# Optimization experiments

Hardware: AMD Instinct MI355X
Metric: run time of the kernel (lower is better)

## Reference

```python
import jax, jax.numpy as jnp
import numpy as np

N_NODES = 100000
N_EDGES = 1600000
IN_DIM = 128
HID_DIM = 128
OUT_DIM = 16
N_GRAPHS = 128


def setup_inputs() -> dict:
    key = jax.random.key(0)
    ks = jax.random.split(key, 8)
    x = jax.random.normal(ks[0], (N_NODES, IN_DIM), dtype=jnp.float32)
    edge_index = jax.random.randint(ks[1], (2, N_EDGES), 0, N_NODES, dtype=jnp.int64)
    batch = jnp.sort(jax.random.randint(ks[2], (N_NODES,), 0, N_GRAPHS, dtype=jnp.int64))
    # GCNConv params (glorot-ish scale) and Linear params
    w1 = jax.random.normal(ks[3], (IN_DIM, HID_DIM), dtype=jnp.float32) / np.sqrt(IN_DIM)
    b1 = jnp.zeros((HID_DIM,), dtype=jnp.float32)
    w2 = jax.random.normal(ks[4], (HID_DIM, HID_DIM), dtype=jnp.float32) / np.sqrt(HID_DIM)
    b2 = jnp.zeros((HID_DIM,), dtype=jnp.float32)
    wc = jax.random.normal(ks[5], (HID_DIM, OUT_DIM), dtype=jnp.float32) / np.sqrt(HID_DIM)
    bc = jnp.zeros((OUT_DIM,), dtype=jnp.float32)
    return {"x": x, "edge_index": edge_index, "batch": batch,
            "w1": w1, "b1": b1, "w2": w2, "b2": b2, "wc": wc, "bc": bc}


def _gcn_layer(h, src, dst, w, b, n_nodes):
    # h: [N, Fin]; src/dst: [E+N] (self-loops already appended)
    h = h @ w  # [N, Fout]
    ones = jnp.ones_like(dst, dtype=h.dtype)
    deg = jax.ops.segment_sum(ones, dst, num_segments=n_nodes)  # [N]
    dinv = jnp.where(deg > 0, jax.lax.rsqrt(deg), 0.0)
    norm = dinv[src] * dinv[dst]  # [E+N]
    msg = h[src] * norm[:, None]  # gather + scale, [E+N, Fout]
    out = jax.ops.segment_sum(msg, dst, num_segments=n_nodes)  # scatter-add
    return out + b


def reference(x, edge_index, batch, w1, b1, w2, b2, wc, bc):
    n = x.shape[0]
    loop = jnp.arange(n, dtype=edge_index.dtype)
    src = jnp.concatenate([edge_index[0], loop])  # add self-loops (PyG default)
    dst = jnp.concatenate([edge_index[1], loop])

    h = jax.nn.relu(_gcn_layer(x, src, dst, w1, b1, n))
    h = jax.nn.relu(_gcn_layer(h, src, dst, w2, b2, n))

    # global mean pool over graphs
    sums = jax.ops.segment_sum(h, batch, num_segments=N_GRAPHS)  # [G, H]
    cnt = jax.ops.segment_sum(jnp.ones((n,), h.dtype), batch, num_segments=N_GRAPHS)
    pooled = sums / jnp.maximum(cnt, 1.0)[:, None]

    return pooled @ wc + bc  # [G, OUT_DIM]
```

## Files before the change

kernel.cpp:

```cpp
#include <hip/hip_runtime.h>
#include <stdint.h>

#define NN 100000
#define NE 1600000
#define FDIM 128
#define NGRAPH 128
#define ODIM 16
#define NBKT 391
#define CAP 4608
#define SCHUNK 4096
#define NSCAT ((NE + SCHUNK - 1) / SCHUNK)

typedef __attribute__((ext_vector_type(8))) short short8;
typedef __attribute__((ext_vector_type(8))) unsigned short ushort8;
typedef __attribute__((ext_vector_type(4))) float f32x4;

__device__ __forceinline__ float blo(unsigned int p) { return __uint_as_float(p << 16); }
__device__ __forceinline__ float bhi(unsigned int p) { return __uint_as_float(p & 0xffff0000u); }
__device__ __forceinline__ unsigned short f2b(float f) {
    unsigned int u = __float_as_uint(f);
    unsigned int r = (u + 0x7fffu + ((u >> 16) & 1u)) >> 16;
    return (unsigned short)r;
}
__device__ __forceinline__ unsigned int packbf(float lo, float hi) {
    return (unsigned int)f2b(lo) | ((unsigned int)f2b(hi) << 16);
}

__device__ __forceinline__ int ld_idx(const int* __restrict__ p, long long i, int w) {
    return w ? p[2 * i] : p[i];
}

__global__ void k_init(const int* __restrict__ ei, int* __restrict__ flag,
                       int* __restrict__ bcursor) {
    __shared__ int s;
    int t = threadIdx.x;
    if (t == 0) s = 0;
    __syncthreads();
    if (t < 64) {
        int v = ei[2 * t + 1];
        if (v != 0) atomicOr(&s, 1);
    }
    if (t < NBKT) bcursor[t] = t * CAP;
    __syncthreads();
    if (t == 0) *flag = (s == 0) ? 1 : 0;
}

__global__ void __launch_bounds__(512) k_scat(const int* __restrict__ ei,
                                              int* __restrict__ bcursor,
                                              unsigned int* __restrict__ rec,
                                              const int* __restrict__ flag) {
    __shared__ int hist[NBKT];
    __shared__ int gcur[NBKT];
    int t = threadIdx.x;
    for (int i = t; i < NBKT; i += 512) hist[i] = 0;
    __syncthreads();
    int w = *flag;
    long long e0 = (long long)blockIdx.x * SCHUNK;
    unsigned int myrec[8];
    int mybkt[8];
    #pragma unroll
    for (int j = 0; j < 8; ++j) {
        long long e = e0 + j * 512 + t;
        if (e < NE) {
            int s = ld_idx(ei, e, w);
            int d = ld_idx(ei, NE + e, w);
            mybkt[j] = d >> 8;
            myrec[j] = (unsigned int)s | ((unsigned int)(d & 255) << 17);
            atomicAdd(&hist[mybkt[j]], 1);
        } else mybkt[j] = -1;
    }
    __syncthreads();
    for (int i = t; i < NBKT; i += 512) {
        int c = hist[i];
        if (c) gcur[i] = atomicAdd(&bcursor[i], c);
    }
    __syncthreads();
    #pragma unroll
    for (int j = 0; j < 8; ++j) {
        int b = mybkt[j];
        if (b >= 0) {
            int p = atomicAdd(&gcur[b], 1);
            if (p < (b + 1) * CAP) rec[p] = myrec[j];
        }
    }
}

__global__ void __launch_bounds__(256) k_bucket(const unsigned int* __restrict__ rec,
                                                const int* __restrict__ bcursor,
                                                int* __restrict__ csr,
                                                int* __restrict__ offs,
                                                int* __restrict__ deg,
                                                float* __restrict__ dinv) {
    __shared__ unsigned int rbuf[CAP];
    __shared__ int srcout[CAP];
    __shared__ int hist[256], scn[256], cur[256];
    int b = blockIdx.x, t = threadIdx.x;
    int base = b * CAP;
    int cnt = bcursor[b] - base;
    if (cnt > CAP) cnt = CAP;
    hist[t] = 0;
    __syncthreads();
    for (int j = t; j < cnt; j += 256) {
        unsigned int r = rec[base + j];
        rbuf[j] = r;
        atomicAdd(&hist[r >> 17], 1);
    }
    __syncthreads();
    int v = hist[t];
    scn[t] = v;
    __syncthreads();
    for (int o = 1; o < 256; o <<= 1) {
        int tv = (t >= o) ? scn[t - o] : 0;
        __syncthreads();
        scn[t] += tv;
        __syncthreads();
    }
    int excl = scn[t] - v;
    cur[t] = excl;
    int node = (b << 8) + t;
    if (node < NN) {
        offs[node] = base + excl;
        deg[node] = v;
        dinv[node] = rsqrtf((float)(v + 1));
    }
    __syncthreads();
    for (int j = t; j < cnt; j += 256) {
        unsigned int r = rbuf[j];
        int p = atomicAdd(&cur[r >> 17], 1);
        srcout[p] = (int)(r & 0x1FFFFu);
    }
    __syncthreads();
    for (int j = t; j < cnt; j += 256) csr[base + j] = srcout[j];
}

__global__ void k_starts(const int* __restrict__ batch, int* __restrict__ gstart,
                         const int* __restrict__ flag) {
    int i = blockIdx.x * 256 + threadIdx.x;
    if (i >= NN) return;
    int w = *flag;
    int b = ld_idx(batch, i, w);
    int prev = (i == 0) ? -1 : ld_idx(batch, i - 1, w);
    for (int g = prev + 1; g <= b; ++g) gstart[g] = i;
    if (i == NN - 1)
        for (int g = b + 1; g <= NGRAPH; ++g) gstart[g] = NN;
}

__global__ void k_transpose(const float* __restrict__ w1, const float* __restrict__ w2,
                            unsigned short* __restrict__ wt1, unsigned short* __restrict__ wt2) {
    int idx = blockIdx.x * 256 + threadIdx.x;
    int which = idx >> 14, r = idx & 16383;
    int k = r >> 7, j = r & 127;
    const float* w = which ? w2 : w1;
    unsigned short* wt = which ? wt2 : wt1;
    wt[j * 128 + k] = f2b(w[k * 128 + j]);
}

#define LWS 136
template <bool BF16IN>
__global__ void __launch_bounds__(256) k_gemm(
    const void* __restrict__ Xv,
    const unsigned short* __restrict__ WT,
    const float* __restrict__ dinv,
    unsigned short* __restrict__ OUT)
{
    __shared__ unsigned short lw[128 * LWS];
    int tid = threadIdx.x;
    for (int it = 0; it < 8; ++it) {
        int vidx = it * 256 + tid;
        int j = vidx >> 4, kc = vidx & 15;
        ushort8 v = *(const ushort8*)(WT + j * 128 + kc * 8);
        *(ushort8*)(&lw[j * LWS + kc * 8]) = v;
    }
    __syncthreads();

    int wave = tid >> 6, lane = tid & 63;
    int quad = lane >> 4, n16 = lane & 15;
    int row0 = (blockIdx.x * 4 + wave) * 16;
    if (row0 >= NN) return;

    f32x4 acc[8];
    for (int ct = 0; ct < 8; ++ct) acc[ct] = (f32x4){0.f, 0.f, 0.f, 0.f};

    const int arow = row0 + n16;
    for (int kk = 0; kk < 4; ++kk) {
        short8 a;
        if (BF16IN) {
            a = *(const short8*)((const unsigned short*)Xv + (size_t)arow * 128 + kk * 32 + quad * 8);
        } else {
            const float* ap = (const float*)Xv + (size_t)arow * 128 + kk * 32 + quad * 8;
            float4 a01 = *(const float4*)(ap);
            float4 a23 = *(const float4*)(ap + 4);
            a[0] = (short)f2b(a01.x); a[1] = (short)f2b(a01.y);
            a[2] = (short)f2b(a01.z); a[3] = (short)f2b(a01.w);
            a[4] = (short)f2b(a23.x); a[5] = (short)f2b(a23.y);
            a[6] = (short)f2b(a23.z); a[7] = (short)f2b(a23.w);
        }
        for (int ct = 0; ct < 8; ++ct) {
            short8 b = *(const short8*)(&lw[(ct * 16 + n16) * LWS + kk * 32 + quad * 8]);
            acc[ct] = __builtin_amdgcn_mfma_f32_16x16x32_bf16(a, b, acc[ct], 0, 0, 0);
        }
    }
    for (int r = 0; r < 4; ++r) {
        int row = row0 + quad * 4 + r;
        float dv = dinv[row];
        for (int ct = 0; ct < 8; ++ct)
            OUT[(size_t)row * 128 + ct * 16 + n16] = f2b(acc[ct][r] * dv);
    }
}

__global__ void __launch_bounds__(256) k_agg(
    const unsigned short* __restrict__ XWS,
    const int* __restrict__ csr,
    const int* __restrict__ offs,
    const int* __restrict__ deg,
    const float* __restrict__ dinv,
    const float* __restrict__ bias,
    unsigned short* __restrict__ H)
{
    int wave = threadIdx.x >> 6, lane = threadIdx.x & 63;
    int v = blockIdx.x * 4 + wave;
    int g = lane >> 4, f = lane & 15;
    int beg = offs[v], end = beg + deg[v];
    float a[8];
    if (g == 0) {
        uint4 q = *(const uint4*)(XWS + (size_t)v * FDIM + f * 8);
        a[0] = blo(q.x); a[1] = bhi(q.x); a[2] = blo(q.y); a[3] = bhi(q.y);
        a[4] = blo(q.z); a[5] = bhi(q.z); a[6] = blo(q.w); a[7] = bhi(q.w);
    } else {
        #pragma unroll
        for (int i = 0; i < 8; ++i) a[i] = 0.f;
    }
    int j = beg;
    for (; j + 4 <= end; j += 4) {
        int idx = csr[j + g];
        uint4 q = *(const uint4*)(XWS + (size_t)idx * FDIM + f * 8);
        a[0] += blo(q.x); a[1] += bhi(q.x); a[2] += blo(q.y); a[3] += bhi(q.y);
        a[4] += blo(q.z); a[5] += bhi(q.z); a[6] += blo(q.w); a[7] += bhi(q.w);
    }
    int rem = end - j;
    if (g < rem) {
        int idx = csr[j + g];
        uint4 q = *(const uint4*)(XWS + (size_t)idx * FDIM + f * 8);
        a[0] += blo(q.x); a[1] += bhi(q.x); a[2] += blo(q.y); a[3] += bhi(q.y);
        a[4] += blo(q.z); a[5] += bhi(q.z); a[6] += blo(q.w); a[7] += bhi(q.w);
    }
    #pragma unroll
    for (int i = 0; i < 8; ++i) {
        a[i] += __shfl_xor(a[i], 16);
        a[i] += __shfl_xor(a[i], 32);
    }
    if (g == 0) {
        float dv = dinv[v];
        float4 b0 = *(const float4*)(bias + f * 8);
        float4 b1 = *(const float4*)(bias + f * 8 + 4);
        uint4 o;
        o.x = packbf(fmaxf(fmaf(a[0], dv, b0.x), 0.f), fmaxf(fmaf(a[1], dv, b0.y), 0.f));
        o.y = packbf(fmaxf(fmaf(a[2], dv, b0.z), 0.f), fmaxf(fmaf(a[3], dv, b0.w), 0.f));
        o.z = packbf(fmaxf(fmaf(a[4], dv, b1.x), 0.f), fmaxf(fmaf(a[5], dv, b1.y), 0.f));
        o.w = packbf(fmaxf(fmaf(a[6], dv, b1.z), 0.f), fmaxf(fmaf(a[7], dv, b1.w), 0.f));
        *(uint4*)(H + (size_t)v * FDIM + f * 8) = o;
    }
}

__global__ void __launch_bounds__(256) k_pool(
    const unsigned short* __restrict__ H, const int* __restrict__ gstart,
    float* __restrict__ pooled)
{
    __shared__ float red[512];
    int g = blockIdx.x;
    int t = threadIdx.x;
    int pair = t & 63;
    int seg = t >> 6;
    int beg = gstart[g], end = gstart[g + 1];
    float a0 = 0.f, a1 = 0.f;
    for (int i = beg + seg; i < end; i += 4) {
        unsigned int q = *(const unsigned int*)(H + (size_t)i * FDIM + 2 * pair);
        a0 += blo(q); a1 += bhi(q);
    }
    red[t] = a0; red[256 + t] = a1;
    __syncthreads();
    if (seg == 0) {
        a0 = red[t] + red[t + 64] + red[t + 128] + red[t + 192];
        a1 = red[256 + t] + red[256 + t + 64] + red[256 + t + 128] + red[256 + t + 192];
        float inv = 1.f / fmaxf((float)(end - beg), 1.f);
        pooled[g * FDIM + 2 * pair]     = a0 * inv;
        pooled[g * FDIM + 2 * pair + 1] = a1 * inv;
    }
}

__global__ void k_cls(const float* __restrict__ pooled, const float* __restrict__ wc,
                      const float* __restrict__ bcb, float* __restrict__ out)
{
    int idx = blockIdx.x * 256 + threadIdx.x;
    if (idx >= NGRAPH * ODIM) return;
    int g = idx >> 4, o = idx & 15;
    float acc = bcb[o];
    for (int f = 0; f < FDIM; ++f)
        acc += pooled[g * FDIM + f] * wc[f * ODIM + o];
    out[idx] = acc;
}

extern "C" void kernel_launch(void* const* d_in, const int* in_sizes, int n_in,
                              void* d_out, int out_size, void* d_ws, size_t ws_size,
                              hipStream_t stream) {
    const float* x   = (const float*)d_in[0];
    const int* ei    = (const int*)d_in[1];
    const int* batch = (const int*)d_in[2];
    const float* w1  = (const float*)d_in[3];
    const float* b1  = (const float*)d_in[4];
    const float* w2  = (const float*)d_in[5];
    const float* b2  = (const float*)d_in[6];
    const float* wc  = (const float*)d_in[7];
    const float* bc  = (const float*)d_in[8];
    float* out = (float*)d_out;

    char* ws = (char*)d_ws;
    size_t off = 0;
    auto alloc = [&](size_t bytes) -> void* {
        off = (off + 255) & ~(size_t)255;
        void* p = ws + off;
        off += bytes;
        return p;
    };
    int*   flag    = (int*)alloc(4);
    int*   bcursor = (int*)alloc(NBKT * 4);
    int*   offs    = (int*)alloc(NN * 4);
    int*   deg     = (int*)alloc(NN * 4);
    float* dinv    = (float*)alloc(NN * 4);
    int*   gstart  = (int*)alloc((NGRAPH + 1) * 4);
    unsigned int* rec = (unsigned int*)alloc((size_t)NBKT * CAP * 4);
    int*   csr     = (int*)alloc((size_t)NBKT * CAP * 4);
    unsigned short* wt1 = (unsigned short*)alloc(128 * 128 * 2);
    unsigned short* wt2 = (unsigned short*)alloc(128 * 128 * 2);
    float* pooled  = (float*)alloc(NGRAPH * FDIM * 4);
    unsigned short* xws = (unsigned short*)alloc((size_t)NN * FDIM * 2);
    unsigned short* h   = (unsigned short*)alloc((size_t)NN * FDIM * 2);

    k_init<<<1, 512, 0, stream>>>(ei, flag, bcursor);
    k_scat<<<NSCAT, 512, 0, stream>>>(ei, bcursor, rec, flag);
    k_bucket<<<NBKT, 256, 0, stream>>>(rec, bcursor, csr, offs, deg, dinv);
    k_starts<<<(NN + 255) / 256, 256, 0, stream>>>(batch, gstart, flag);
    k_transpose<<<128, 256, 0, stream>>>(w1, w2, wt1, wt2);

    k_gemm<false><<<(NN / 16 + 3) / 4, 256, 0, stream>>>(x, wt1, dinv, xws);
    k_agg<<<NN / 4, 256, 0, stream>>>(xws, csr, offs, deg, dinv, b1, h);
    k_gemm<true><<<(NN / 16 + 3) / 4, 256, 0, stream>>>(h, wt2, dinv, xws);
    k_agg<<<NN / 4, 256, 0, stream>>>(xws, csr, offs, deg, dinv, b2, h);
    k_pool<<<NGRAPH, 256, 0, stream>>>(h, gstart, pooled);
    k_cls<<<8, 256, 0, stream>>>(pooled, wc, bc, out);
}
```

Measured before the change: 365.3 us.

## Split GCN aggregation across feature slices with eight edges per wave

Result: slower. 853.3 us (+133.6%).

```diff
diff --git a/kernel.cpp b/kernel.cpp
--- a/kernel.cpp
+++ b/kernel.cpp
@@ -217,48 +217,34 @@
     const float* __restrict__ bias,
     unsigned short* __restrict__ H)
 {
+    int slice = blockIdx.x & 7;
+    int grp   = blockIdx.x >> 3;
     int wave = threadIdx.x >> 6, lane = threadIdx.x & 63;
-    int v = blockIdx.x * 4 + wave;
-    int g = lane >> 4, f = lane & 15;
+    int v = grp * 4 + wave;
+    int e8 = lane >> 3, dw = lane & 7;
+    int fb = slice * 16 + dw * 2;
     int beg = offs[v], end = beg + deg[v];
-    float a[8];
-    if (g == 0) {
-        uint4 q = *(const uint4*)(XWS + (size_t)v * FDIM + f * 8);
-        a[0] = blo(q.x); a[1] = bhi(q.x); a[2] = blo(q.y); a[3] = bhi(q.y);
-        a[4] = blo(q.z); a[5] = bhi(q.z); a[6] = blo(q.w); a[7] = bhi(q.w);
-    } else {
-        #pragma unroll
-        for (int i = 0; i < 8; ++i) a[i] = 0.f;
-    }
-    int j = beg;
-    for (; j + 4 <= end; j += 4) {
-        int idx = csr[j + g];
-        uint4 q = *(const uint4*)(XWS + (size_t)idx * FDIM + f * 8);
-        a[0] += blo(q.x); a[1] += bhi(q.x); a[2] += blo(q.y); a[3] += bhi(q.y);
-        a[4] += blo(q.z); a[5] += bhi(q.z); a[6] += blo(q.w); a[7] += bhi(q.w);
-    }
-    int rem = end - j;
-    if (g < rem) {
-        int idx = csr[j + g];
-        uint4 q = *(const uint4*)(XWS + (size_t)idx * FDIM + f * 8);
-        a[0] += blo(q.x); a[1] += bhi(q.x); a[2] += blo(q.y); a[3] += bhi(q.y);
-        a[4] += blo(q.z); a[5] += bhi(q.z); a[6] += blo(q.w); a[7] += bhi(q.w);
-    }
-    #pragma unroll
-    for (int i = 0; i < 8; ++i) {
-        a[i] += __shfl_xor(a[i], 16);
-        a[i] += __shfl_xor(a[i], 32);
-    }
-    if (g == 0) {
+    float a0 = 0.f, a1 = 0.f;
+    if (e8 == 0) {
+        unsigned int q = *(const unsigned int*)(XWS + (size_t)v * FDIM + fb);
+        a0 = blo(q); a1 = bhi(q);
+    }
+    for (int j = beg; j < end; j += 8) {
+        int jj = j + e8;
+        if (jj < end) {
+            int idx = csr[jj];
+            unsigned int q = *(const unsigned int*)(XWS + (size_t)idx * FDIM + fb);
+            a0 += blo(q); a1 += bhi(q);
+        }
+    }
+    a0 += __shfl_xor(a0, 8);  a1 += __shfl_xor(a1, 8);
+    a0 += __shfl_xor(a0, 16); a1 += __shfl_xor(a1, 16);
+    a0 += __shfl_xor(a0, 32); a1 += __shfl_xor(a1, 32);
+    if (e8 == 0) {
         float dv = dinv[v];
-        float4 b0 = *(const float4*)(bias + f * 8);
-        float4 b1 = *(const float4*)(bias + f * 8 + 4);
-        uint4 o;
-        o.x = packbf(fmaxf(fmaf(a[0], dv, b0.x), 0.f), fmaxf(fmaf(a[1], dv, b0.y), 0.f));
-        o.y = packbf(fmaxf(fmaf(a[2], dv, b0.z), 0.f), fmaxf(fmaf(a[3], dv, b0.w), 0.f));
-        o.z = packbf(fmaxf(fmaf(a[4], dv, b1.x), 0.f), fmaxf(fmaf(a[5], dv, b1.y), 0.f));
-        o.w = packbf(fmaxf(fmaf(a[6], dv, b1.z), 0.f), fmaxf(fmaf(a[7], dv, b1.w), 0.f));
-        *(uint4*)(H + (size_t)v * FDIM + f * 8) = o;
+        float2 bp = *(const float2*)(bias + fb);
+        *(unsigned int*)(H + (size_t)v * FDIM + fb) =
+            packbf(fmaxf(fmaf(a0, dv, bp.x), 0.f), fmaxf(fmaf(a1, dv, bp.y), 0.f));
     }
 }
 
@@ -343,9 +329,9 @@
     k_transpose<<<128, 256, 0, stream>>>(w1, w2, wt1, wt2);
 
     k_gemm<false><<<(NN / 16 + 3) / 4, 256, 0, stream>>>(x, wt1, dinv, xws);
-    k_agg<<<NN / 4, 256, 0, stream>>>(xws, csr, offs, deg, dinv, b1, h);
+    k_agg<<<(NN / 4) * 8, 256, 0, stream>>>(xws, csr, offs, deg, dinv, b1, h);
     k_gemm<true><<<(NN / 16 + 3) / 4, 256, 0, stream>>>(h, wt2, dinv, xws);
-    k_agg<<<NN / 4, 256, 0, stream>>>(xws, csr, offs, deg, dinv, b2, h);
+    k_agg<<<(NN / 4) * 8, 256, 0, stream>>>(xws, csr, offs, deg, dinv, b2, h);
     k_pool<<<NGRAPH, 256, 0, stream>>>(h, gstart, pooled);
     k_cls<<<8, 256, 0, stream>>>(pooled, wc, bc, out);
 }
```

## Merge setup kernels, fuse pooling with classifier, unroll aggregation gather by two

Applied to the files above, without the earlier changes.

Result: faster. 342.2 us (-6.3%).

```diff
diff --git a/kernel.cpp b/kernel.cpp
--- a/kernel.cpp
+++ b/kernel.cpp
@@ -10,6 +10,7 @@
 #define CAP 4608
 #define SCHUNK 4096
 #define NSCAT ((NE + SCHUNK - 1) / SCHUNK)
+#define NSTARTB ((NN + 255) / 256)
 
 typedef __attribute__((ext_vector_type(8))) short short8;
 typedef __attribute__((ext_vector_type(8))) unsigned short ushort8;
@@ -26,35 +27,54 @@
     return (unsigned int)f2b(lo) | ((unsigned int)f2b(hi) << 16);
 }
 
+__device__ __forceinline__ int detect_w(const int* __restrict__ ei) {
+    int lane = threadIdx.x & 63;
+    int v = ei[2 * lane + 1];
+    return (__ballot(v != 0) == 0ULL) ? 1 : 0;
+}
 __device__ __forceinline__ int ld_idx(const int* __restrict__ p, long long i, int w) {
     return w ? p[2 * i] : p[i];
 }
 
-__global__ void k_init(const int* __restrict__ ei, int* __restrict__ flag,
-                       int* __restrict__ bcursor) {
-    __shared__ int s;
-    int t = threadIdx.x;
-    if (t == 0) s = 0;
-    __syncthreads();
-    if (t < 64) {
-        int v = ei[2 * t + 1];
-        if (v != 0) atomicOr(&s, 1);
-    }
-    if (t < NBKT) bcursor[t] = t * CAP;
-    __syncthreads();
-    if (t == 0) *flag = (s == 0) ? 1 : 0;
+__global__ void __launch_bounds__(256) k_prep(
+    const float* __restrict__ w1, const float* __restrict__ w2,
+    unsigned short* __restrict__ wt1, unsigned short* __restrict__ wt2,
+    const int* __restrict__ ei, const int* __restrict__ batch,
+    int* __restrict__ gstart, int* __restrict__ bcursor)
+{
+    int b = blockIdx.x, t = threadIdx.x;
+    if (b < 128) {
+        int idx = b * 256 + t;
+        int which = idx >> 14, r = idx & 16383;
+        int k = r >> 7, j = r & 127;
+        const float* w = which ? w2 : w1;
+        unsigned short* wt = which ? wt2 : wt1;
+        wt[j * 128 + k] = f2b(w[k * 128 + j]);
+    } else if (b < 128 + NSTARTB) {
+        int w = detect_w(ei);
+        int i = (b - 128) * 256 + t;
+        if (i < NN) {
+            int bb = ld_idx(batch, i, w);
+            int prev = (i == 0) ? -1 : ld_idx(batch, i - 1, w);
+            for (int g = prev + 1; g <= bb; ++g) gstart[g] = i;
+            if (i == NN - 1)
+                for (int g = bb + 1; g <= NGRAPH; ++g) gstart[g] = NN;
+        }
+    } else {
+        int i = (b - 128 - NSTARTB) * 256 + t;
+        if (i < NBKT) bcursor[i] = i * CAP;
+    }
 }
 
 __global__ void __launch_bounds__(512) k_scat(const int* __restrict__ ei,
                                               int* __restrict__ bcursor,
-                                              unsigned int* __restrict__ rec,
-                                              const int* __restrict__ flag) {
+                                              unsigned int* __restrict__ rec) {
     __shared__ int hist[NBKT];
     __shared__ int gcur[NBKT];
     int t = threadIdx.x;
+    int w = detect_w(ei);
     for (int i = t; i < NBKT; i += 512) hist[i] = 0;
     __syncthreads();
-    int w = *flag;
     long long e0 = (long long)blockIdx.x * SCHUNK;
     unsigned int myrec[8];
     int mybkt[8];
@@ -131,28 +151,6 @@
     }
     __syncthreads();
     for (int j = t; j < cnt; j += 256) csr[base + j] = srcout[j];
-}
-
-__global__ void k_starts(const int* __restrict__ batch, int* __restrict__ gstart,
-                         const int* __restrict__ flag) {
-    int i = blockIdx.x * 256 + threadIdx.x;
-    if (i >= NN) return;
-    int w = *flag;
-    int b = ld_idx(batch, i, w);
-    int prev = (i == 0) ? -1 : ld_idx(batch, i - 1, w);
-    for (int g = prev + 1; g <= b; ++g) gstart[g] = i;
-    if (i == NN - 1)
-        for (int g = b + 1; g <= NGRAPH; ++g) gstart[g] = NN;
-}
-
-__global__ void k_transpose(const float* __restrict__ w1, const float* __restrict__ w2,
-                            unsigned short* __restrict__ wt1, unsigned short* __restrict__ wt2) {
-    int idx = blockIdx.x * 256 + threadIdx.x;
-    int which = idx >> 14, r = idx & 16383;
-    int k = r >> 7, j = r & 127;
-    const float* w = which ? w2 : w1;
-    unsigned short* wt = which ? wt2 : wt1;
-    wt[j * 128 + k] = f2b(w[k * 128 + j]);
 }
 
 #define LWS 136
@@ -231,11 +229,21 @@
         for (int i = 0; i < 8; ++i) a[i] = 0.f;
     }
     int j = beg;
-    for (; j + 4 <= end; j += 4) {
+    for (; j + 8 <= end; j += 8) {
+        int i0 = csr[j + g], i1 = csr[j + 4 + g];
+        uint4 q0 = *(const uint4*)(XWS + (size_t)i0 * FDIM + f * 8);
+        uint4 q1 = *(const uint4*)(XWS + (size_t)i1 * FDIM + f * 8);
+        a[0] += blo(q0.x); a[1] += bhi(q0.x); a[2] += blo(q0.y); a[3] += bhi(q0.y);
+        a[4] += blo(q0.z); a[5] += bhi(q0.z); a[6] += blo(q0.w); a[7] += bhi(q0.w);
+        a[0] += blo(q1.x); a[1] += bhi(q1.x); a[2] += blo(q1.y); a[3] += bhi(q1.y);
+        a[4] += blo(q1.z); a[5] += bhi(q1.z); a[6] += blo(q1.w); a[7] += bhi(q1.w);
+    }
+    if (j + 4 <= end) {
         int idx = csr[j + g];
         uint4 q = *(const uint4*)(XWS + (size_t)idx * FDIM + f * 8);
         a[0] += blo(q.x); a[1] += bhi(q.x); a[2] += blo(q.y); a[3] += bhi(q.y);
         a[4] += blo(q.z); a[5] += bhi(q.z); a[6] += blo(q.w); a[7] += bhi(q.w);
+        j += 4;
     }
     int rem = end - j;
     if (g < rem) {
@@ -262,11 +270,13 @@
     }
 }
 
-__global__ void __launch_bounds__(256) k_pool(
+__global__ void __launch_bounds__(256) k_poolcls(
     const unsigned short* __restrict__ H, const int* __restrict__ gstart,
-    float* __restrict__ pooled)
+    const float* __restrict__ wc, const float* __restrict__ bc,
+    float* __restrict__ out)
 {
     __shared__ float red[512];
+    __shared__ float pl[FDIM];
     int g = blockIdx.x;
     int t = threadIdx.x;
     int pair = t & 63;
@@ -283,21 +293,23 @@
         a0 = red[t] + red[t + 64] + red[t + 128] + red[t + 192];
         a1 = red[256 + t] + red[256 + t + 64] + red[256 + t + 128] + red[256 + t + 192];
         float inv = 1.f / fmaxf((float)(end - beg), 1.f);
-        pooled[g * FDIM + 2 * pair]     = a0 * inv;
-        pooled[g * FDIM + 2 * pair + 1] = a1 * inv;
-    }
-}
-
-__global__ void k_cls(const float* __restrict__ pooled, const float* __restrict__ wc,
-                      const float* __restrict__ bcb, float* __restrict__ out)
-{
-    int idx = blockIdx.x * 256 + threadIdx.x;
-    if (idx >= NGRAPH * ODIM) return;
-    int g = idx >> 4, o = idx & 15;
-    float acc = bcb[o];
-    for (int f = 0; f < FDIM; ++f)
-        acc += pooled[g * FDIM + f] * wc[f * ODIM + o];
-    out[idx] = acc;
+        pl[2 * pair] = a0 * inv;
+        pl[2 * pair + 1] = a1 * inv;
+    }
+    __syncthreads();
+    int o = t & 15, fs = t >> 4;
+    float acc = 0.f;
+    #pragma unroll
+    for (int k = 0; k < 8; ++k)
+        acc += pl[fs * 8 + k] * wc[(fs * 8 + k) * ODIM + o];
+    red[t] = acc;
+    __syncthreads();
+    if (t < 16) {
+        float s = bc[t];
+        #pragma unroll
+        for (int k = 0; k < 16; ++k) s += red[k * 16 + t];
+        out[g * ODIM + t] = s;
+    }
 }
 
 extern "C" void kernel_launch(void* const* d_in, const int* in_sizes, int n_in,
@@ -322,7 +334,6 @@
         off += bytes;
         return p;
     };
-    int*   flag    = (int*)alloc(4);
     int*   bcursor = (int*)alloc(NBKT * 4);
     int*   offs    = (int*)alloc(NN * 4);
     int*   deg     = (int*)alloc(NN * 4);
@@ -332,20 +343,16 @@
     int*   csr     = (int*)alloc((size_t)NBKT * CAP * 4);
     unsigned short* wt1 = (unsigned short*)alloc(128 * 128 * 2);
     unsigned short* wt2 = (unsigned short*)alloc(128 * 128 * 2);
-    float* pooled  = (float*)alloc(NGRAPH * FDIM * 4);
     unsigned short* xws = (unsigned short*)alloc((size_t)NN * FDIM * 2);
     unsigned short* h   = (unsigned short*)alloc((size_t)NN * FDIM * 2);
 
-    k_init<<<1, 512, 0, stream>>>(ei, flag, bcursor);
-    k_scat<<<NSCAT, 512, 0, stream>>>(ei, bcursor, rec, flag);
+    k_prep<<<128 + NSTARTB + 2, 256, 0, stream>>>(w1, w2, wt1, wt2, ei, batch, gstart, bcursor);
+    k_scat<<<NSCAT, 512, 0, stream>>>(ei, bcursor, rec);
     k_bucket<<<NBKT, 256, 0, stream>>>(rec, bcursor, csr, offs, deg, dinv);
-    k_starts<<<(NN + 255) / 256, 256, 0, stream>>>(batch, gstart, flag);
-    k_transpose<<<128, 256, 0, stream>>>(w1, w2, wt1, wt2);
 
     k_gemm<false><<<(NN / 16 + 3) / 4, 256, 0, stream>>>(x, wt1, dinv, xws);
     k_agg<<<NN / 4, 256, 0, stream>>>(xws, csr, offs, deg, dinv, b1, h);
     k_gemm<true><<<(NN / 16 + 3) / 4, 256, 0, stream>>>(h, wt2, dinv, xws);
     k_agg<<<NN / 4, 256, 0, stream>>>(xws, csr, offs, deg, dinv, b2, h);
-    k_pool<<<NGRAPH, 256, 0, stream>>>(h, gstart, pooled);
-    k_cls<<<8, 256, 0, stream>>>(pooled, wc, bc, out);
-}
+    k_poolcls<<<NGRAPH, 256, 0, stream>>>(h, gstart, wc, bc, out);
+}
```
